# Kernel optimization log

Measured on AMD Instinct MI355X. Metric: run time of the kernel, lower is better.

## Reference

```python
import jax, jax.numpy as jnp
import numpy as np

CLAMP_LO, CLAMP_HI, CLAMP_GATE_MAX = -10.0, 10.0, 10.0
E, TOPK = 8, 2
M, K, N = 2048, 2048, 1408  # tokens, hidden_dim, intermediate_dim
CAPACITY = 2 * (M * TOPK // E)


def setup_inputs() -> dict:
    key = jax.random.key(0)
    ks = jax.random.split(key, 6)
    bk = 1.0 / np.sqrt(K)  # kaiming_uniform(a=sqrt(5)) bound = 1/sqrt(fan_in)
    bn = 1.0 / np.sqrt(N)
    return {
        "flat_h": jax.random.normal(ks[0], (M, K), jnp.float32),
        "flat_idx": jax.random.randint(ks[1], (M, TOPK), 0, E),
        "flat_gate": jax.random.uniform(ks[2], (M, TOPK), jnp.float32),
        "gate_weight": jax.random.uniform(ks[3], (E, N, K), jnp.float32, -bk, bk),
        "up_weight": jax.random.uniform(ks[4], (E, N, K), jnp.float32, -bk, bk),
        "down_weight": jax.random.uniform(ks[5], (E, K, N), jnp.float32, -bn, bn),
    }


def reference(flat_h, flat_idx, flat_gate, gate_weight, up_weight, down_weight):
    m, top_k = flat_idx.shape
    k = flat_h.shape[1]
    e = gate_weight.shape[0]
    r = m * top_k

    expert_id = flat_idx.reshape(-1)                                   # (R,)
    gate = flat_gate.reshape(-1)                                       # (R,)
    token_index = jnp.repeat(jnp.arange(m, dtype=jnp.int32), top_k)    # (R,)

    # stable sort rows by expert id (mirrors torch.argsort(..., stable=True))
    sort_idx = jnp.argsort(expert_id, stable=True)
    sorted_eid = expert_id[sort_idx]
    tok_sorted = token_index[sort_idx]
    gate_sorted = gate[sort_idx]

    # position of each sorted row inside its expert group
    counts = jnp.bincount(expert_id, length=e)
    starts = jnp.concatenate([jnp.zeros(1, counts.dtype), jnp.cumsum(counts)[:-1]])
    pos = jnp.arange(r) - starts[sorted_eid]                           # (R,)

    # dispatch: scatter sorted tokens into fixed-capacity (E, C, K) buffer
    buf = jnp.zeros((e, CAPACITY, k), flat_h.dtype)
    buf = buf.at[sorted_eid, pos].set(flat_h[tok_sorted])

    # grouped GEMMs: weights stored (E, out, in) like nn.Linear
    g = jnp.einsum("eck,enk->ecn", buf, gate_weight)
    g = jnp.minimum(g, CLAMP_GATE_MAX)
    u = jnp.clip(jnp.einsum("eck,enk->ecn", buf, up_weight), CLAMP_LO, CLAMP_HI)
    h = jax.nn.silu(g) * u                                             # SwiGLU (E, C, N)
    d = jnp.einsum("ecn,ekn->eck", h, down_weight)                     # (E, C, K)

    # combine: gather each routed row back, weight by gate, sum over top_k slots
    expert_out = d[sorted_eid, pos]                                    # (R, K)
    weighted = expert_out * gate_sorted[:, None]
    out = jnp.zeros((m, k), flat_h.dtype).at[tok_sorted].add(weighted)
    return out
```

## Files before the change

### kernel.cpp

```cpp
#include <hip/hip_runtime.h>
#include <hip/hip_bf16.h>

#define M_TOK 2048
#define KDIM 2048
#define NDIM 1408
#define NEXP 8
#define RROWS (M_TOK * 2)
#define CAP 1024

typedef __attribute__((ext_vector_type(8))) short short8;
typedef __attribute__((ext_vector_type(4))) float f32x4;

__device__ __forceinline__ unsigned short bf16rn(float f) {
    unsigned int u = __builtin_bit_cast(unsigned int, f);
    u += 0x7FFFu + ((u >> 16) & 1u);
    return (unsigned short)(u >> 16);
}
__device__ __forceinline__ unsigned int pk2(float a, float b) {
    return (unsigned int)bf16rn(a) | ((unsigned int)bf16rn(b) << 16);
}
__device__ __forceinline__ unsigned int cvtpk(float a, float b) {
    __hip_bfloat162 h = __float22bfloat162_rn(make_float2(a, b));
    unsigned int u;
    __builtin_memcpy(&u, &h, 4);
    return u;
}

__device__ __forceinline__ void glds16(const void* g, void* l) {
    __builtin_amdgcn_global_load_lds(
        (const __attribute__((address_space(1))) unsigned int*)g,
        (__attribute__((address_space(3))) unsigned int*)l, 16, 0, 0);
}

__global__ void k_route(const float* __restrict__ h, const int* __restrict__ idx,
                        int* __restrict__ cnt, int* __restrict__ slot_of,
                        unsigned short* __restrict__ bufA) {
    int r = blockIdx.x;
    __shared__ int s_ep;
    if (threadIdx.x == 0) {
        int e = idx[r];
        int p = atomicAdd(&cnt[e], 1);
        int ep = e * CAP + p;
        slot_of[r] = ep;
        s_ep = ep;
    }
    __syncthreads();
    int ep = s_ep;
    const float4* src = (const float4*)(h + (size_t)(r >> 1) * KDIM) + threadIdx.x * 2;
    float4 a = src[0], b = src[1];
    uint4 o;
    o.x = pk2(a.x, a.y); o.y = pk2(a.z, a.w);
    o.z = pk2(b.x, b.y); o.w = pk2(b.z, b.w);
    *((uint4*)(bufA + (size_t)ep * KDIM) + threadIdx.x) = o;
}

__global__ __launch_bounds__(256, 2)
void k_gemm1(const unsigned short* __restrict__ bufA,
             const float* __restrict__ gw,
             const float* __restrict__ uw,
             const int* __restrict__ cnt, unsigned short* __restrict__ hbuf) {
    const int f = blockIdx.x;
    const int e = f & 7;
    const int t = f >> 3;
    const int n_blk = t % 11;
    const int m_blk = t / 11;
    const int m0 = m_blk * 128;
    if (m0 >= cnt[e]) return;
    const int n0 = n_blk * 128;

    const unsigned short* A = bufA + (size_t)e * CAP * KDIM;
    const float* G = gw + (size_t)e * NDIM * KDIM;
    const float* U = uw + (size_t)e * NDIM * KDIM;

    __shared__ unsigned short sA[128 * 64];
    __shared__ unsigned short sG[128 * 64];
    __shared__ unsigned short sU[128 * 64];

    const int tid = threadIdx.x;
    const int lane = tid & 63;
    const int wave = tid >> 6;
    const int wm = (wave >> 1) * 64, wn = (wave & 1) * 64;
    const int q = lane >> 4, l15 = lane & 15;
    const int sr = lane >> 3;
    const int scb = (lane & 7) ^ (sr & 7);
    const int xi = l15 & 7;
    const int cbl0 = (q ^ xi) * 8;
    const int cbl1 = ((4 + q) ^ xi) * 8;

    const int row_t = tid >> 4;
    const int c4 = tid & 15;
    const float* Gb = G + (size_t)(n0 + row_t) * KDIM + c4 * 4;
    const float* Ub = U + (size_t)(n0 + row_t) * KDIM + c4 * 4;
    const int swz = (((c4 >> 1) ^ (row_t & 7)) << 3) + ((c4 & 1) << 2);
    unsigned short* wpG = &sG[row_t * 64 + swz];
    unsigned short* wpU = &sU[row_t * 64 + swz];

    f32x4 accG[4][4] = {};
    f32x4 accU[4][4] = {};

    float4 gv[8], uv[8];
#pragma unroll
    for (int i = 0; i < 8; i++) gv[i] = *(const float4*)(Gb + (size_t)i * 16 * KDIM);
#pragma unroll
    for (int i = 0; i < 8; i++) uv[i] = *(const float4*)(Ub + (size_t)i * 16 * KDIM);

    for (int k0 = 0; k0 < KDIM; k0 += 64) {
        __syncthreads();
#pragma unroll
        for (int i = 0; i < 8; i++) {
            uint2 o;
            o.x = cvtpk(gv[i].x, gv[i].y);
            o.y = cvtpk(gv[i].z, gv[i].w);
            *(uint2*)(wpG + i * 1024) = o;
        }
#pragma unroll
        for (int i = 0; i < 8; i++) {
            uint2 o;
            o.x = cvtpk(uv[i].x, uv[i].y);
            o.y = cvtpk(uv[i].z, uv[i].w);
            *(uint2*)(wpU + i * 1024) = o;
        }
#pragma unroll
        for (int c = 0; c < 4; c++) {
            int seg = wave * 4 + c;
            int row = seg * 8 + sr;
            glds16(A + (size_t)(m0 + row) * KDIM + k0 + scb * 8, &sA[seg * 512]);
        }
        if (k0 + 64 < KDIM) {
            const float* Gn = Gb + k0 + 64;
            const float* Un = Ub + k0 + 64;
#pragma unroll
            for (int i = 0; i < 8; i++) gv[i] = *(const float4*)(Gn + (size_t)i * 16 * KDIM);
#pragma unroll
            for (int i = 0; i < 8; i++) uv[i] = *(const float4*)(Un + (size_t)i * 16 * KDIM);
        }
        __syncthreads();

#pragma unroll
        for (int kh = 0; kh < 2; kh++) {
            const int co = kh ? cbl1 : cbl0;
            short8 af[4], gf[4], uf[4];
#pragma unroll
            for (int i = 0; i < 4; i++) {
                af[i] = *(const short8*)&sA[(wm + i * 16 + l15) * 64 + co];
                gf[i] = *(const short8*)&sG[(wn + i * 16 + l15) * 64 + co];
                uf[i] = *(const short8*)&sU[(wn + i * 16 + l15) * 64 + co];
            }
#pragma unroll
            for (int i = 0; i < 4; i++)
#pragma unroll
                for (int j = 0; j < 4; j++) {
                    accG[i][j] = __builtin_amdgcn_mfma_f32_16x16x32_bf16(af[i], gf[j], accG[i][j], 0, 0, 0);
                    accU[i][j] = __builtin_amdgcn_mfma_f32_16x16x32_bf16(af[i], uf[j], accU[i][j], 0, 0, 0);
                }
        }
    }

    unsigned short* H = hbuf + (size_t)e * CAP * NDIM;
#pragma unroll
    for (int i = 0; i < 4; i++)
#pragma unroll
        for (int j = 0; j < 4; j++) {
            int col = n0 + wn + j * 16 + l15;
#pragma unroll
            for (int rg = 0; rg < 4; rg++) {
                int row = m0 + wm + i * 16 + q * 4 + rg;
                float g = accG[i][j][rg];
                float u = accU[i][j][rg];
                g = fminf(g, 10.f);
                u = fminf(fmaxf(u, -10.f), 10.f);
                float hv = g / (1.f + __expf(-g)) * u;
                H[(size_t)row * NDIM + col] = bf16rn(hv);
            }
        }
}

__global__ __launch_bounds__(256, 2)
void k_gemm2(const unsigned short* __restrict__ hbuf,
             const float* __restrict__ dwn, const int* __restrict__ cnt,
             float* __restrict__ dbuf) {
    const int f = blockIdx.x;
    const int e = f & 7;
    const int t = f >> 3;
    const int n_blk = t & 15;
    const int m_blk = t >> 4;
    const int cnt_e = cnt[e];
    const int m0 = m_blk * 128;
    if (m0 >= cnt_e) return;
    const int n0 = n_blk * 128;

    const unsigned short* A = hbuf + (size_t)e * CAP * NDIM;
    const float* B = dwn + (size_t)e * KDIM * NDIM;

    __shared__ unsigned short sA[128 * 64];
    __shared__ unsigned short sB[128 * 64];

    const int tid = threadIdx.x;
    const int lane = tid & 63;
    const int wave = tid >> 6;
    const int wm = (wave >> 1) * 64, wn = (wave & 1) * 64;
    const int q = lane >> 4, l15 = lane & 15;
    const int sr = lane >> 3;
    const int scb = (lane & 7) ^ (sr & 7);
    const int xi = l15 & 7;
    const int cbl0 = (q ^ xi) * 8;
    const int cbl1 = ((4 + q) ^ xi) * 8;

    const int row_t = tid >> 4;
    const int c4 = tid & 15;
    const float* Bb = B + (size_t)(n0 + row_t) * NDIM + c4 * 4;
    const int swz = (((c4 >> 1) ^ (row_t & 7)) << 3) + ((c4 & 1) << 2);
    unsigned short* wpB = &sB[row_t * 64 + swz];

    f32x4 acc[4][4] = {};

    float4 bv[8];
#pragma unroll
    for (int i = 0; i < 8; i++) bv[i] = *(const float4*)(Bb + (size_t)i * 16 * NDIM);

    for (int k0 = 0; k0 < NDIM; k0 += 64) {
        __syncthreads();
#pragma unroll
        for (int i = 0; i < 8; i++) {
            uint2 o;
            o.x = cvtpk(bv[i].x, bv[i].y);
            o.y = cvtpk(bv[i].z, bv[i].w);
            *(uint2*)(wpB + i * 1024) = o;
        }
#pragma unroll
        for (int c = 0; c < 4; c++) {
            int seg = wave * 4 + c;
            int row = seg * 8 + sr;
            glds16(A + (size_t)(m0 + row) * NDIM + k0 + scb * 8, &sA[seg * 512]);
        }
        if (k0 + 64 < NDIM) {
            const float* Bn = Bb + k0 + 64;
#pragma unroll
            for (int i = 0; i < 8; i++) bv[i] = *(const float4*)(Bn + (size_t)i * 16 * NDIM);
        }
        __syncthreads();

#pragma unroll
        for (int kh = 0; kh < 2; kh++) {
            const int co = kh ? cbl1 : cbl0;
            short8 af[4], bfr[4];
#pragma unroll
            for (int i = 0; i < 4; i++) {
                af[i] = *(const short8*)&sA[(wm + i * 16 + l15) * 64 + co];
                bfr[i] = *(const short8*)&sB[(wn + i * 16 + l15) * 64 + co];
            }
#pragma unroll
            for (int i = 0; i < 4; i++)
#pragma unroll
                for (int j = 0; j < 4; j++)
                    acc[i][j] = __builtin_amdgcn_mfma_f32_16x16x32_bf16(af[i], bfr[j], acc[i][j], 0, 0, 0);
        }
    }

    float* D = dbuf + (size_t)e * CAP * KDIM;
#pragma unroll
    for (int i = 0; i < 4; i++) {
#pragma unroll
        for (int rg = 0; rg < 4; rg++) {
            int row = m0 + wm + i * 16 + q * 4 + rg;
            if (row < cnt_e) {
                float* drow = D + (size_t)row * KDIM + n0 + wn + l15;
#pragma unroll
                for (int j = 0; j < 4; j++)
                    drow[j * 16] = acc[i][j][rg];
            }
        }
    }
}

__global__ void k_combine(const float* __restrict__ dbuf, const int* __restrict__ slot_of,
                          const float* __restrict__ gate, float* __restrict__ out) {
    int tk = blockIdx.x;
    int s0 = slot_of[2 * tk], s1 = slot_of[2 * tk + 1];
    float g0 = gate[2 * tk], g1 = gate[2 * tk + 1];
    const float4* r0 = (const float4*)(dbuf + (size_t)s0 * KDIM);
    const float4* r1 = (const float4*)(dbuf + (size_t)s1 * KDIM);
    float4* o = (float4*)(out + (size_t)tk * KDIM);
    int i = threadIdx.x * 2;
#pragma unroll
    for (int c = 0; c < 2; c++) {
        float4 a = r0[i + c], b = r1[i + c];
        float4 v;
        v.x = g0 * a.x + g1 * b.x;
        v.y = g0 * a.y + g1 * b.y;
        v.z = g0 * a.z + g1 * b.z;
        v.w = g0 * a.w + g1 * b.w;
        o[i + c] = v;
    }
}

extern "C" void kernel_launch(void* const* d_in, const int* in_sizes, int n_in,
                              void* d_out, int out_size, void* d_ws, size_t ws_size,
                              hipStream_t stream) {
    const float* flat_h = (const float*)d_in[0];
    const int* flat_idx = (const int*)d_in[1];
    const float* flat_gate = (const float*)d_in[2];
    const float* gw = (const float*)d_in[3];
    const float* uw = (const float*)d_in[4];
    const float* dwn = (const float*)d_in[5];
    float* out = (float*)d_out;

    char* w = (char*)d_ws;
    int* cnt = (int*)w;
    int* slot_of = (int*)(w + 256);
    unsigned short* bufA = (unsigned short*)(w + 1048576ull);
    unsigned short* hbuf = (unsigned short*)(w + 34603008ull);
    float* dbuf = (float*)(w + 57671680ull);

    hipMemsetAsync(cnt, 0, 256, stream);

    k_route<<<RROWS, 256, 0, stream>>>(flat_h, flat_idx, cnt, slot_of, bufA);
    k_gemm1<<<8 * 11 * 8, 256, 0, stream>>>(bufA, gw, uw, cnt, hbuf);
    k_gemm2<<<8 * 16 * 8, 256, 0, stream>>>(hbuf, dwn, cnt, dbuf);
    k_combine<<<M_TOK, 256, 0, stream>>>(dbuf, slot_of, flat_gate, out);
}
```

Baseline: 461.4 us.

## Double-buffer A tile in LDS with async prefetch in both expert GEMMs

Adds a second LDS buffer for the bf16 activation tile in both grouped GEMM kernels, so the direct global-to-LDS load of the next K-slice is issued one iteration ahead and overlaps the current MFMA work. The __syncthreads calls are replaced by raw s_barrier plus explicit vmcnt/lgkmcnt waits and sched_barriers. This is meant to hide activation load latency, at the cost of extra LDS (four 16KB arrays in gemm1), which may reduce occupancy. The vmcnt(0) wait placed after the barrier also stalls on the freshly issued prefetch, which could cancel much of the intended overlap.

```diff
diff --git a/kernel.cpp b/kernel.cpp
--- a/kernel.cpp
+++ b/kernel.cpp
@@ -72,7 +72,8 @@
     const float* G = gw + (size_t)e * NDIM * KDIM;
     const float* U = uw + (size_t)e * NDIM * KDIM;
 
-    __shared__ unsigned short sA[128 * 64];
+    __shared__ unsigned short sA0[128 * 64];
+    __shared__ unsigned short sA1[128 * 64];
     __shared__ unsigned short sG[128 * 64];
     __shared__ unsigned short sU[128 * 64];
 
@@ -98,14 +99,26 @@
     f32x4 accG[4][4] = {};
     f32x4 accU[4][4] = {};
 
+    unsigned short* sAr = sA0;
+    unsigned short* sAw = sA1;
+
     float4 gv[8], uv[8];
 #pragma unroll
+    for (int c = 0; c < 4; c++) {
+        int seg = wave * 4 + c;
+        int row = seg * 8 + sr;
+        glds16(A + (size_t)(m0 + row) * KDIM + scb * 8, &sA0[seg * 512]);
+    }
+#pragma unroll
     for (int i = 0; i < 8; i++) gv[i] = *(const float4*)(Gb + (size_t)i * 16 * KDIM);
 #pragma unroll
     for (int i = 0; i < 8; i++) uv[i] = *(const float4*)(Ub + (size_t)i * 16 * KDIM);
 
     for (int k0 = 0; k0 < KDIM; k0 += 64) {
-        __syncthreads();
+        __builtin_amdgcn_s_barrier();
+        asm volatile("s_waitcnt vmcnt(0)" ::: "memory");
+        __builtin_amdgcn_sched_barrier(0);
+
 #pragma unroll
         for (int i = 0; i < 8; i++) {
             uint2 o;
@@ -120,13 +133,14 @@
             o.y = cvtpk(uv[i].z, uv[i].w);
             *(uint2*)(wpU + i * 1024) = o;
         }
-#pragma unroll
-        for (int c = 0; c < 4; c++) {
-            int seg = wave * 4 + c;
-            int row = seg * 8 + sr;
-            glds16(A + (size_t)(m0 + row) * KDIM + k0 + scb * 8, &sA[seg * 512]);
-        }
+
         if (k0 + 64 < KDIM) {
+#pragma unroll
+            for (int c = 0; c < 4; c++) {
+                int seg = wave * 4 + c;
+                int row = seg * 8 + sr;
+                glds16(A + (size_t)(m0 + row) * KDIM + k0 + 64 + scb * 8, &sAw[seg * 512]);
+            }
             const float* Gn = Gb + k0 + 64;
             const float* Un = Ub + k0 + 64;
 #pragma unroll
@@ -134,7 +148,10 @@
 #pragma unroll
             for (int i = 0; i < 8; i++) uv[i] = *(const float4*)(Un + (size_t)i * 16 * KDIM);
         }
-        __syncthreads();
+
+        asm volatile("s_waitcnt lgkmcnt(0)" ::: "memory");
+        __builtin_amdgcn_sched_barrier(0);
+        __builtin_amdgcn_s_barrier();
 
 #pragma unroll
         for (int kh = 0; kh < 2; kh++) {
@@ -142,7 +159,7 @@
             short8 af[4], gf[4], uf[4];
 #pragma unroll
             for (int i = 0; i < 4; i++) {
-                af[i] = *(const short8*)&sA[(wm + i * 16 + l15) * 64 + co];
+                af[i] = *(const short8*)&sAr[(wm + i * 16 + l15) * 64 + co];
                 gf[i] = *(const short8*)&sG[(wn + i * 16 + l15) * 64 + co];
                 uf[i] = *(const short8*)&sU[(wn + i * 16 + l15) * 64 + co];
             }
@@ -154,6 +171,8 @@
                     accU[i][j] = __builtin_amdgcn_mfma_f32_16x16x32_bf16(af[i], uf[j], accU[i][j], 0, 0, 0);
                 }
         }
+
+        unsigned short* tmp = sAr; sAr = sAw; sAw = tmp;
     }
 
     unsigned short* H = hbuf + (size_t)e * CAP * NDIM;
@@ -192,7 +211,8 @@
     const unsigned short* A = hbuf + (size_t)e * CAP * NDIM;
     const float* B = dwn + (size_t)e * KDIM * NDIM;
 
-    __shared__ unsigned short sA[128 * 64];
+    __shared__ unsigned short sA0[128 * 64];
+    __shared__ unsigned short sA1[128 * 64];
     __shared__ unsigned short sB[128 * 64];
 
     const int tid = threadIdx.x;
@@ -214,12 +234,24 @@
 
     f32x4 acc[4][4] = {};
 
+    unsigned short* sAr = sA0;
+    unsigned short* sAw = sA1;
+
     float4 bv[8];
 #pragma unroll
+    for (int c = 0; c < 4; c++) {
+        int seg = wave * 4 + c;
+        int row = seg * 8 + sr;
+        glds16(A + (size_t)(m0 + row) * NDIM + scb * 8, &sA0[seg * 512]);
+    }
+#pragma unroll
     for (int i = 0; i < 8; i++) bv[i] = *(const float4*)(Bb + (size_t)i * 16 * NDIM);
 
     for (int k0 = 0; k0 < NDIM; k0 += 64) {
-        __syncthreads();
+        __builtin_amdgcn_s_barrier();
+        asm volatile("s_waitcnt vmcnt(0)" ::: "memory");
+        __builtin_amdgcn_sched_barrier(0);
+
 #pragma unroll
         for (int i = 0; i < 8; i++) {
             uint2 o;
@@ -227,18 +259,22 @@
             o.y = cvtpk(bv[i].z, bv[i].w);
             *(uint2*)(wpB + i * 1024) = o;
         }
-#pragma unroll
-        for (int c = 0; c < 4; c++) {
-            int seg = wave * 4 + c;
-            int row = seg * 8 + sr;
-            glds16(A + (size_t)(m0 + row) * NDIM + k0 + scb * 8, &sA[seg * 512]);
-        }
+
         if (k0 + 64 < NDIM) {
+#pragma unroll
+            for (int c = 0; c < 4; c++) {
+                int seg = wave * 4 + c;
+                int row = seg * 8 + sr;
+                glds16(A + (size_t)(m0 + row) * NDIM + k0 + 64 + scb * 8, &sAw[seg * 512]);
+            }
             const float* Bn = Bb + k0 + 64;
 #pragma unroll
             for (int i = 0; i < 8; i++) bv[i] = *(const float4*)(Bn + (size_t)i * 16 * NDIM);
         }
-        __syncthreads();
+
+        asm volatile("s_waitcnt lgkmcnt(0)" ::: "memory");
+        __builtin_amdgcn_sched_barrier(0);
+        __builtin_amdgcn_s_barrier();
 
 #pragma unroll
         for (int kh = 0; kh < 2; kh++) {
@@ -246,7 +282,7 @@
             short8 af[4], bfr[4];
 #pragma unroll
             for (int i = 0; i < 4; i++) {
-                af[i] = *(const short8*)&sA[(wm + i * 16 + l15) * 64 + co];
+                af[i] = *(const short8*)&sAr[(wm + i * 16 + l15) * 64 + co];
                 bfr[i] = *(const short8*)&sB[(wn + i * 16 + l15) * 64 + co];
             }
 #pragma unroll
@@ -255,6 +291,8 @@
                 for (int j = 0; j < 4; j++)
                     acc[i][j] = __builtin_amdgcn_mfma_f32_16x16x32_bf16(af[i], bfr[j], acc[i][j], 0, 0, 0);
         }
+
+        unsigned short* tmp = sAr; sAr = sAw; sAw = tmp;
     }
 
     float* D = dbuf + (size_t)e * CAP * KDIM;
```

Measured after the change: 431.9 us. 1.07x faster.
